# Kernel optimization log

Measured on AMD Instinct MI355X. Metric: run time of the kernel, lower is better.

The kernel has to match this reference:

```python
import jax, jax.numpy as jnp
import numpy as np
from itertools import combinations

H_RANK_MAX = 2
TP_RANK_MAX = 2
BASIS_RANK_MAX = 2
DIM = 3
N_NODES = 50000
N_EDGES = 400000
N_CHANNELS = 16
R_CUT = 10.0  # radial cutoff for Bessel RBF (assumed)


def find_combinations(a_max, b_max, s):
    if s > a_max + b_max or s < 0:
        return []
    return [(a, s - a) for a in range(max(0, s - b_max), min(a_max, s) + 1)]


def contraction_is_valid(n_in, n_out):
    # legs are removed in pairs (Kronecker-delta contractions)
    return (n_in >= n_out) and ((n_in - n_out) % 2 == 0)


def _matchings(legs):
    # all perfect matchings of an even-size list of leg indices
    if not legs:
        yield []
        return
    a = legs[0]
    for i in range(1, len(legs)):
        rest = legs[1:i] + legs[i + 1:]
        for m in _matchings(rest):
            yield [(a, legs[i])] + m


def contraction_specs(a, b, c_out):
    # all einsum strings contracting an [E,K,dim^a] x [E,K,dim^b] tensor product
    # (a+b legs total) down to c_out free Cartesian legs, pairing the rest.
    n = a + b
    specs = []
    for free in combinations(range(n), c_out):
        paired = [i for i in range(n) if i not in free]
        for m in _matchings(paired):
            lbl = {}
            it = iter('mnopqrstuvwxyz')
            for f in free:
                lbl[f] = next(it)
            for (i, j) in m:
                L = next(it)
                lbl[i] = L
                lbl[j] = L
            sa = ''.join(lbl[i] for i in range(a))
            sb = ''.join(lbl[i] for i in range(a, n))
            so = ''.join(lbl[f] for f in free)
            specs.append(f'ek{sa},ek{sb}->ek{so}')
    return specs


def e_rbf(r, n):
    # Bessel radial basis: n is [K,1], r is [E] -> [K,E]
    return jnp.sqrt(2.0 / R_CUT) * jnp.sin(n * jnp.pi * r / R_CUT) / r


def tensor_prod(r, order):
    # repeated outer product of unit vectors: order 0 -> [E], order k -> [E] + [DIM]*k
    out = jnp.ones(r.shape[0], dtype=r.dtype)
    for _ in range(order):
        out = jnp.einsum('e...,ed->e...d', out, r)
    return out


def setup_inputs() -> dict:
    key = jax.random.key(0)
    ks = jax.random.split(key, 7)
    h0 = jax.random.normal(ks[0], (N_NODES, N_CHANNELS), jnp.float32)
    h1 = jax.random.normal(ks[1], (N_NODES, N_CHANNELS, DIM), jnp.float32)
    h2 = jax.random.normal(ks[2], (N_NODES, N_CHANNELS, DIM, DIM), jnp.float32)
    pos = jax.random.normal(ks[3], (N_NODES, DIM), jnp.float32)
    channel_weights = jax.random.normal(ks[4], (H_RANK_MAX + 1, N_CHANNELS, N_CHANNELS), jnp.float32)
    src = jax.random.randint(ks[5], (N_EDGES,), 0, N_NODES, dtype=jnp.int32)
    off = jax.random.randint(ks[6], (N_EDGES,), 1, N_NODES, dtype=jnp.int32)
    dst = (src + off) % N_NODES  # no self-loops -> no zero distances
    edge_index = jnp.stack([src, dst])
    return {"h0": h0, "h1": h1, "h2": h2, "pos": pos,
            "channel_weights": channel_weights, "edge_index": edge_index}


def reference(h0, h1, h2, pos, channel_weights, edge_index):
    h = [h0, h1, h2]
    src, dst = edge_index[0], edge_index[1]
    rel = pos[src] - pos[dst]                       # [E,3]
    dists = jnp.linalg.norm(rel, axis=-1)           # [E]
    unit = rel / dists[:, None]
    hg = [g[dst] for g in h]                        # per-edge gathered features
    # NOTE: the original forward computes channel-mixed self.h with channel_weights
    # but the contraction loop uses the UNMIXED gathered h (h[split[0]]); replicated here,
    # so channel_weights does not affect the output (zero gradient).
    n_vals = jnp.arange(1, N_CHANNELS + 1, dtype=dists.dtype)[:, None]  # [K,1]
    radial = e_rbf(dists, n_vals).reshape(N_EDGES, N_CHANNELS)  # faithful reshape (not transpose), as in source
    r_raw = [tensor_prod(unit, o) for o in range(TP_RANK_MAX + 1)]
    r_w = [jnp.einsum('ek,e...->ek...', radial, t) for t in r_raw]  # [E,K]+[3]*b
    outs = [None] * (BASIS_RANK_MAX + 1)
    for n_ind in range(H_RANK_MAX + TP_RANK_MAX + 1):
        for (a, b) in find_combinations(H_RANK_MAX, TP_RANK_MAX, n_ind):
            for br in range(BASIS_RANK_MAX + 1):
                if contraction_is_valid(n_ind, br):
                    for spec in contraction_specs(a, b, br):
                        t = jnp.einsum(spec, hg[a], r_w[b])
                        outs[br] = t if outs[br] is None else outs[br] + t
    # sum over paths (done incrementally above == stack + 'i...->...'), scatter to nodes
    res = []
    for t in outs:
        if t is not None:
            res.append(jax.ops.segment_sum(t, src, num_segments=N_NODES))
    return tuple(res)
```

## Files before the change

### kernel.cpp

```cpp
#include <hip/hip_runtime.h>
#include <math.h>

#define N_NODES   50000
#define N_EDGES   400000
#define NCH       16
#define CAP       48
#define NSTRIPE   8
#define TPB       256
#define NBN       ((N_NODES + TPB - 1) / TPB)
#define NB_EDGES  ((N_EDGES + TPB - 1) / TPB)


__global__ void build_kernel(const float* __restrict__ pos,
                             const int* __restrict__ src,
                             const int* __restrict__ dst,
                             float* __restrict__ dists,
                             int* __restrict__ cnt,
                             int2* __restrict__ ebuf) {
    int e = blockIdx.x * TPB + threadIdx.x;
    if (e >= N_EDGES) return;
    int s = src[e];
    int d = dst[e];
    float rx = pos[3 * s + 0] - pos[3 * d + 0];
    float ry = pos[3 * s + 1] - pos[3 * d + 1];
    float rz = pos[3 * s + 2] - pos[3 * d + 2];
    float dist = sqrtf(rx * rx + ry * ry + rz * rz);
    dists[e] = dist;
    int slot = atomicAdd(&cnt[s], 1);
    if (slot < CAP) {
        ebuf[s * CAP + slot] = make_int2(e, d);
    }
}

__device__ __forceinline__ void edge_math(
    float ux, float uy, float uz, float R,
    float A0, const float A1[3], const float A2[9],
    float& acc0, float acc1[3], float acc2[9])
{
    float u[3] = {ux, uy, uz};
    float d1 = A1[0] * ux + A1[1] * uy + A1[2] * uz;
    float tA = A2[0] + A2[4] + A2[8];
    float v0 = A2[0] * ux + A2[1] * uy + A2[2] * uz;
    float v1 = A2[3] * ux + A2[4] * uy + A2[5] * uz;
    float v2 = A2[6] * ux + A2[7] * uy + A2[8] * uz;
    float w0 = A2[0] * ux + A2[3] * uy + A2[6] * uz;
    float w1 = A2[1] * ux + A2[4] * uy + A2[7] * uz;
    float w2 = A2[2] * ux + A2[5] * uy + A2[8] * uz;
    float q = ux * v0 + uy * v1 + uz * v2;

    acc0 += R * (2.0f * A0 + d1 + 2.0f * tA + 2.0f * q);

    float svw[3] = {v0 + w0, v1 + w1, v2 + w2};
    float a0t = A0 + tA;
#pragma unroll
    for (int mm = 0; mm < 3; ++mm) {
        acc1[mm] += R * (A0 * u[mm] + 2.0f * A1[mm] + 2.0f * d1 * u[mm]
                         + svw[mm] + tA * u[mm]);
#pragma unroll
        for (int nn = 0; nn < 3; ++nn) {
            acc2[3 * mm + nn] += R * (a0t * u[mm] * u[nn] + A1[mm] * u[nn]
                                      + 2.0f * A2[3 * mm + nn]
                                      + 2.0f * svw[mm] * u[nn]);
        }
    }
}

__device__ __forceinline__ void load_hset(
    const float* __restrict__ h0, const float* __restrict__ h1,
    const float* __restrict__ h2, const float* __restrict__ dists,
    int d, int e, int k,
    float& A0, float A1[3], float A2[9], float& r, float& nf)
{
    A0 = h0[d * NCH + k];
    const float* p1 = h1 + ((size_t)d * NCH + k) * 3;
    A1[0] = p1[0]; A1[1] = p1[1]; A1[2] = p1[2];
    const float* p2 = h2 + ((size_t)d * NCH + k) * 9;
#pragma unroll
    for (int q2 = 0; q2 < 9; ++q2) A2[q2] = p2[q2];
    unsigned f = (unsigned)e * NCH + (unsigned)k;
    unsigned n_idx = f / (unsigned)N_EDGES;
    unsigned e_idx = f - n_idx * (unsigned)N_EDGES;
    r = dists[e_idx];
    nf = (float)(n_idx + 1);
}

__device__ __forceinline__ float radial_R(float nf, float r) {
    return 0.44721359549995794f * __sinf(nf * 0.3141592653589793f * r) / r;
}

__global__ void node_wave_fast(const float* __restrict__ h0,
                               const float* __restrict__ h1,
                               const float* __restrict__ h2,
                               const float* __restrict__ pos,
                               const int* __restrict__ cnt,
                               const int2* __restrict__ ebuf,
                               const float* __restrict__ dists,
                               float* __restrict__ out0,
                               float* __restrict__ out1,
                               float* __restrict__ out2) {
    int gid = blockIdx.x * TPB + threadIdx.x;
    int node = gid >> 6;
    if (node >= N_NODES) return;
    int lane = threadIdx.x & 63;
    int k = lane & 15;
    int j = lane >> 4;
    int base = node * CAP;

    int m = cnt[node];
    int2 pk = ebuf[base + j];
    float ps0 = pos[3 * node + 0];
    float ps1 = pos[3 * node + 1];
    float ps2 = pos[3 * node + 2];
    if (m > CAP) m = CAP;

    float acc0 = 0.0f;
    float acc1[3] = {0.0f, 0.0f, 0.0f};
    float acc2[9] = {0.0f, 0.0f, 0.0f, 0.0f, 0.0f, 0.0f, 0.0f, 0.0f, 0.0f};

    int c = j;
    while (c < m) {
        int cn = c + 4;
        int2 pkn = pk;
        if (cn < m) pkn = ebuf[base + cn];

        int e = pk.x;
        int d = pk.y;

        float pd0 = pos[3 * d + 0];
        float pd1 = pos[3 * d + 1];
        float pd2 = pos[3 * d + 2];

        float A0 = h0[d * NCH + k];
        const float* a1p = h1 + ((size_t)d * NCH + k) * 3;
        float A1[3] = {a1p[0], a1p[1], a1p[2]};
        const float* a2p = h2 + ((size_t)d * NCH + k) * 9;
        float A2[9];
#pragma unroll
        for (int q2 = 0; q2 < 9; ++q2) A2[q2] = a2p[q2];

        unsigned f = (unsigned)e * NCH + (unsigned)k;
        unsigned n_idx = f / (unsigned)N_EDGES;
        unsigned e_idx = f - n_idx * (unsigned)N_EDGES;
        float r = dists[e_idx];
        float R = 0.44721359549995794f *
                  __sinf((float)(n_idx + 1) * 0.3141592653589793f * r) / r;

        float rx = ps0 - pd0;
        float ry = ps1 - pd1;
        float rz = ps2 - pd2;
        float dist = sqrtf(rx * rx + ry * ry + rz * rz);
        float inv = 1.0f / dist;
        float ux = rx * inv, uy = ry * inv, uz = rz * inv;

        edge_math(ux, uy, uz, R, A0, A1, A2, acc0, acc1, acc2);

        pk = pkn;
        c = cn;
    }

    acc0 += __shfl_xor(acc0, 16, 64);
    acc0 += __shfl_xor(acc0, 32, 64);
#pragma unroll
    for (int mm = 0; mm < 3; ++mm) {
        acc1[mm] += __shfl_xor(acc1[mm], 16, 64);
        acc1[mm] += __shfl_xor(acc1[mm], 32, 64);
    }
#pragma unroll
    for (int mm = 0; mm < 9; ++mm) {
        acc2[mm] += __shfl_xor(acc2[mm], 16, 64);
        acc2[mm] += __shfl_xor(acc2[mm], 32, 64);
    }

    if (j == 0) {
        int t = node * NCH + k;
        out0[t] = acc0;
        float* o1p = out1 + (size_t)t * 3;
#pragma unroll
        for (int mm = 0; mm < 3; ++mm) o1p[mm] = acc1[mm];
        float* o2p = out2 + (size_t)t * 9;
#pragma unroll
        for (int mm = 0; mm < 9; ++mm) o2p[mm] = acc2[mm];
    }
}


__global__ void fb_geom_hist(const float* __restrict__ pos,
                             const int* __restrict__ src,
                             const int* __restrict__ dst,
                             float* __restrict__ dists,
                             int* __restrict__ cnt8,
                             int* __restrict__ rankArr) {
    int e = blockIdx.x * TPB + threadIdx.x;
    if (e >= N_EDGES) return;
    int stripe = blockIdx.x & (NSTRIPE - 1);
    int s = src[e];
    int d = dst[e];
    float rx = pos[3 * s + 0] - pos[3 * d + 0];
    float ry = pos[3 * s + 1] - pos[3 * d + 1];
    float rz = pos[3 * s + 2] - pos[3 * d + 2];
    dists[e] = sqrtf(rx * rx + ry * ry + rz * rz);
    rankArr[e] = atomicAdd(&cnt8[stripe * N_NODES + s], 1);
}

__global__ void fb_scan(const int* __restrict__ cnt8,
                        int* __restrict__ incl,
                        int* __restrict__ bsum) {
    __shared__ int sh[TPB];
    int tid = threadIdx.x;
    int i = blockIdx.x * TPB + tid;
    int tot = 0;
    if (i < N_NODES) {
#pragma unroll
        for (int c = 0; c < NSTRIPE; ++c) tot += cnt8[c * N_NODES + i];
    }
    sh[tid] = tot;
    __syncthreads();
    for (int s = 1; s < TPB; s <<= 1) {
        int x = 0;
        if (tid >= s) x = sh[tid - s];
        __syncthreads();
        if (tid >= s) sh[tid] += x;
        __syncthreads();
    }
    if (i < N_NODES) incl[i] = sh[tid];
    if (tid == TPB - 1) bsum[blockIdx.x] = sh[TPB - 1];
}

__global__ void fb_final(const int* __restrict__ cnt8,
                         const int* __restrict__ incl,
                         const int* __restrict__ bsum,
                         int* __restrict__ offsets,
                         int* __restrict__ copyBase) {
    __shared__ int sh[TPB];
    int tid = threadIdx.x;
    int b = blockIdx.x;
    sh[tid] = (tid < b) ? bsum[tid] : 0;
    __syncthreads();
    for (int s = 128; s > 0; s >>= 1) {
        if (tid < s) sh[tid] += sh[tid + s];
        __syncthreads();
    }
    int base = sh[0];
    int i = b * TPB + tid;
    if (i < N_NODES) {
        int cv[NSTRIPE];
        int tot = 0;
#pragma unroll
        for (int c = 0; c < NSTRIPE; ++c) { cv[c] = cnt8[c * N_NODES + i]; tot += cv[c]; }
        int off = base + incl[i] - tot;
        offsets[i] = off;
        int run = off;
#pragma unroll
        for (int c = 0; c < NSTRIPE; ++c) { copyBase[c * N_NODES + i] = run; run += cv[c]; }
    }
    if (b == 0 && tid == 0) offsets[N_NODES] = N_EDGES;
}

__global__ void fb_fill(const int* __restrict__ src,
                        const int* __restrict__ dst,
                        const float* __restrict__ pos,
                        const float* __restrict__ dists,
                        const int* __restrict__ copyBase,
                        const int* __restrict__ rankArr,
                        float4* __restrict__ edata,
                        int* __restrict__ csr) {
    int e = blockIdx.x * TPB + threadIdx.x;
    if (e >= N_EDGES) return;
    int stripe = blockIdx.x & (NSTRIPE - 1);
    int s = src[e];
    int d = dst[e];
    float rx = pos[3 * s + 0] - pos[3 * d + 0];
    float ry = pos[3 * s + 1] - pos[3 * d + 1];
    float rz = pos[3 * s + 2] - pos[3 * d + 2];
    float inv = 1.0f / dists[e];
    int slot = copyBase[stripe * N_NODES + s] + rankArr[e];
    float4 ed;
    ed.x = rx * inv;
    ed.y = ry * inv;
    ed.z = rz * inv;
    ed.w = __int_as_float(d);
    edata[slot] = ed;
    csr[slot] = e;
}

__global__ void fb_main(const float* __restrict__ h0,
                        const float* __restrict__ h1,
                        const float* __restrict__ h2,
                        const int* __restrict__ offsets,
                        const float4* __restrict__ edata,
                        const int* __restrict__ csr,
                        const float* __restrict__ dists,
                        float* __restrict__ out0,
                        float* __restrict__ out1,
                        float* __restrict__ out2) {
    int gid = blockIdx.x * TPB + threadIdx.x;
    int node = gid >> 6;
    if (node >= N_NODES) return;
    int lane = threadIdx.x & 63;
    int k = lane & 15;
    int j = lane >> 4;
    int beg = offsets[node];
    int end = offsets[node + 1];

    float acc0 = 0.0f;
    float acc1[3] = {0.0f, 0.0f, 0.0f};
    float acc2[9] = {0.0f, 0.0f, 0.0f, 0.0f, 0.0f, 0.0f, 0.0f, 0.0f, 0.0f};

    int i = beg + j;
    float4 ed;
    int e = 0;
    if (i < end) { ed = edata[i]; e = csr[i]; }
    while (i < end) {
        int inext = i + 4;
        float4 edn = ed;
        int en = e;
        if (inext < end) { edn = edata[inext]; en = csr[inext]; }

        int d = __float_as_int(ed.w);
        float a0, a1[3], a2[9], r, nf;
        load_hset(h0, h1, h2, dists, d, e, k, a0, a1, a2, r, nf);
        float R = radial_R(nf, r);
        edge_math(ed.x, ed.y, ed.z, R, a0, a1, a2, acc0, acc1, acc2);

        ed = edn;
        e = en;
        i = inext;
    }

    acc0 += __shfl_xor(acc0, 16, 64);
    acc0 += __shfl_xor(acc0, 32, 64);
#pragma unroll
    for (int mm = 0; mm < 3; ++mm) {
        acc1[mm] += __shfl_xor(acc1[mm], 16, 64);
        acc1[mm] += __shfl_xor(acc1[mm], 32, 64);
    }
#pragma unroll
    for (int mm = 0; mm < 9; ++mm) {
        acc2[mm] += __shfl_xor(acc2[mm], 16, 64);
        acc2[mm] += __shfl_xor(acc2[mm], 32, 64);
    }

    if (j == 0) {
        int t = node * NCH + k;
        out0[t] = acc0;
        float* o1p = out1 + (size_t)t * 3;
#pragma unroll
        for (int mm = 0; mm < 3; ++mm) o1p[mm] = acc1[mm];
        float* o2p = out2 + (size_t)t * 9;
#pragma unroll
        for (int mm = 0; mm < 9; ++mm) o2p[mm] = acc2[mm];
    }
}


extern "C" void kernel_launch(void* const* d_in, const int* in_sizes, int n_in,
                              void* d_out, int out_size, void* d_ws, size_t ws_size,
                              hipStream_t stream) {
    const float* h0  = (const float*)d_in[0];
    const float* h1  = (const float*)d_in[1];
    const float* h2  = (const float*)d_in[2];
    const float* pos = (const float*)d_in[3];
    const int* edge_index = (const int*)d_in[5];
    const int* src = edge_index;
    const int* dst = edge_index + N_EDGES;

    float* out = (float*)d_out;
    float* out0 = out;
    float* out1 = out + (size_t)N_NODES * NCH;
    float* out2 = out + (size_t)N_NODES * NCH * 4;

    size_t need = (size_t)N_NODES * CAP * 8 + (size_t)N_EDGES * 4 + (size_t)N_NODES * 4;

    if (ws_size >= need) {
        int2* ebuf   = (int2*)d_ws;
        float* dists = (float*)(ebuf + (size_t)N_NODES * CAP);
        int* cnt     = (int*)(dists + N_EDGES);

        hipMemsetAsync(cnt, 0, N_NODES * sizeof(int), stream);
        build_kernel<<<NB_EDGES, TPB, 0, stream>>>(pos, src, dst, dists, cnt, ebuf);
        node_wave_fast<<<(N_NODES * 64 + TPB - 1) / TPB, TPB, 0, stream>>>(
            h0, h1, h2, pos, cnt, ebuf, dists, out0, out1, out2);
    } else {
        float4* edata   = (float4*)d_ws;
        float*  dists   = (float*)(edata + N_EDGES);
        int* cnt8       = (int*)(dists + N_EDGES);
        int* rankArr    = cnt8 + NSTRIPE * N_NODES;
        int* incl       = rankArr + N_EDGES;
        int* bsum       = incl + N_NODES;
        int* offsets    = bsum + 256;
        int* copyBase   = offsets + N_NODES + 1;
        int* csr        = copyBase + NSTRIPE * N_NODES;

        hipMemsetAsync(cnt8, 0, NSTRIPE * N_NODES * sizeof(int), stream);
        fb_geom_hist<<<NB_EDGES, TPB, 0, stream>>>(pos, src, dst, dists, cnt8, rankArr);
        fb_scan<<<NBN, TPB, 0, stream>>>(cnt8, incl, bsum);
        fb_final<<<NBN, TPB, 0, stream>>>(cnt8, incl, bsum, offsets, copyBase);
        fb_fill<<<NB_EDGES, TPB, 0, stream>>>(src, dst, pos, dists, copyBase, rankArr, edata, csr);
        fb_main<<<(N_NODES * 64 + TPB - 1) / TPB, TPB, 0, stream>>>(
            h0, h1, h2, offsets, edata, csr, dists, out0, out1, out2);
    }
}
```

Measured before the change: 184.4 us.

## Pack two nodes per wavefront and software-pipeline neighbor gathers

The main node kernel now processes two nodes per 64-lane wavefront (2 edge slots × 16 channels per node instead of 4), halving the grid and the shuffle reduction depth. The edge loop is software-pipelined: the next edge's position, h features and distance are loaded before the current edge's math runs, with unconditional ebuf reads made safe by padding the buffer. Division and sqrt are replaced by hardware rcp/rsq approximations. This targets gather latency and idle lanes for low-degree nodes, at the cost of more registers and fewer parallel edge slots per node.

```diff
diff --git a/kernel.cpp b/kernel.cpp
--- a/kernel.cpp
+++ b/kernel.cpp
@@ -5,10 +5,12 @@
 #define N_EDGES   400000
 #define NCH       16
 #define CAP       48
+#define EBUF_PAD  16
 #define NSTRIPE   8
 #define TPB       256
 #define NBN       ((N_NODES + TPB - 1) / TPB)
 #define NB_EDGES  ((N_EDGES + TPB - 1) / TPB)
+#define NB_MAIN   ((N_NODES / 2 * 64) / TPB)
 
 
 __global__ void build_kernel(const float* __restrict__ pos,
@@ -65,6 +67,30 @@
     }
 }
 
+__device__ __forceinline__ void load_hsetp(
+    const float* __restrict__ h0, const float* __restrict__ h1,
+    const float* __restrict__ h2, const float* __restrict__ pos,
+    const float* __restrict__ dists,
+    int d, int e, int k,
+    float& P0, float& P1, float& P2,
+    float& A0, float A1[3], float A2[9], float& r, float& nf)
+{
+    P0 = pos[3 * d + 0];
+    P1 = pos[3 * d + 1];
+    P2 = pos[3 * d + 2];
+    A0 = h0[d * NCH + k];
+    const float* p1 = h1 + ((size_t)d * NCH + k) * 3;
+    A1[0] = p1[0]; A1[1] = p1[1]; A1[2] = p1[2];
+    const float* p2 = h2 + ((size_t)d * NCH + k) * 9;
+#pragma unroll
+    for (int q2 = 0; q2 < 9; ++q2) A2[q2] = p2[q2];
+    unsigned f = (unsigned)e * NCH + (unsigned)k;
+    unsigned n_idx = f / (unsigned)N_EDGES;
+    unsigned e_idx = f - n_idx * (unsigned)N_EDGES;
+    r = dists[e_idx];
+    nf = (float)(n_idx + 1);
+}
+
 __device__ __forceinline__ void load_hset(
     const float* __restrict__ h0, const float* __restrict__ h1,
     const float* __restrict__ h2, const float* __restrict__ dists,
@@ -99,77 +125,67 @@
                                float* __restrict__ out1,
                                float* __restrict__ out2) {
     int gid = blockIdx.x * TPB + threadIdx.x;
-    int node = gid >> 6;
+    int lane = threadIdx.x & 63;
+    int half = lane >> 5;
+    int j = (lane >> 4) & 1;
+    int k = lane & 15;
+    int node = (gid >> 6) * 2 + half;
     if (node >= N_NODES) return;
-    int lane = threadIdx.x & 63;
-    int k = lane & 15;
-    int j = lane >> 4;
     int base = node * CAP;
 
     int m = cnt[node];
-    int2 pk = ebuf[base + j];
     float ps0 = pos[3 * node + 0];
     float ps1 = pos[3 * node + 1];
     float ps2 = pos[3 * node + 2];
+    int c = j;
+    int2 pk = ebuf[base + c];
     if (m > CAP) m = CAP;
+
+    bool v0 = (c < m);
+    int dc = v0 ? pk.y : 0;
+    int ec = v0 ? pk.x : 0;
+    float pd0, pd1, pd2, A0, A1[3], A2[9], rr, nf;
+    load_hsetp(h0, h1, h2, pos, dists, dc, ec, k,
+               pd0, pd1, pd2, A0, A1, A2, rr, nf);
 
     float acc0 = 0.0f;
     float acc1[3] = {0.0f, 0.0f, 0.0f};
     float acc2[9] = {0.0f, 0.0f, 0.0f, 0.0f, 0.0f, 0.0f, 0.0f, 0.0f, 0.0f};
 
-    int c = j;
     while (c < m) {
-        int cn = c + 4;
-        int2 pkn = pk;
-        if (cn < m) pkn = ebuf[base + cn];
-
-        int e = pk.x;
-        int d = pk.y;
-
-        float pd0 = pos[3 * d + 0];
-        float pd1 = pos[3 * d + 1];
-        float pd2 = pos[3 * d + 2];
-
-        float A0 = h0[d * NCH + k];
-        const float* a1p = h1 + ((size_t)d * NCH + k) * 3;
-        float A1[3] = {a1p[0], a1p[1], a1p[2]};
-        const float* a2p = h2 + ((size_t)d * NCH + k) * 9;
-        float A2[9];
-#pragma unroll
-        for (int q2 = 0; q2 < 9; ++q2) A2[q2] = a2p[q2];
-
-        unsigned f = (unsigned)e * NCH + (unsigned)k;
-        unsigned n_idx = f / (unsigned)N_EDGES;
-        unsigned e_idx = f - n_idx * (unsigned)N_EDGES;
-        float r = dists[e_idx];
+        int cn = c + 2;
+        int2 pk1 = ebuf[base + cn];
+        bool vn = (cn < m);
+        int dn = vn ? pk1.y : 0;
+        int en = vn ? pk1.x : 0;
+        float qd0, qd1, qd2, B0, B1[3], B2[9], sr, snf;
+        load_hsetp(h0, h1, h2, pos, dists, dn, en, k,
+                   qd0, qd1, qd2, B0, B1, B2, sr, snf);
+
+        float rcp_r = __builtin_amdgcn_rcpf(rr);
         float R = 0.44721359549995794f *
-                  __sinf((float)(n_idx + 1) * 0.3141592653589793f * r) / r;
-
+                  __sinf(nf * 0.3141592653589793f * rr) * rcp_r;
         float rx = ps0 - pd0;
         float ry = ps1 - pd1;
         float rz = ps2 - pd2;
-        float dist = sqrtf(rx * rx + ry * ry + rz * rz);
-        float inv = 1.0f / dist;
-        float ux = rx * inv, uy = ry * inv, uz = rz * inv;
-
-        edge_math(ux, uy, uz, R, A0, A1, A2, acc0, acc1, acc2);
-
-        pk = pkn;
+        float s2 = rx * rx + ry * ry + rz * rz;
+        float inv = __builtin_amdgcn_rsqf(s2);
+        edge_math(rx * inv, ry * inv, rz * inv, R, A0, A1, A2, acc0, acc1, acc2);
+
+        pd0 = qd0; pd1 = qd1; pd2 = qd2;
+        A0 = B0;
+        A1[0] = B1[0]; A1[1] = B1[1]; A1[2] = B1[2];
+#pragma unroll
+        for (int q2 = 0; q2 < 9; ++q2) A2[q2] = B2[q2];
+        rr = sr; nf = snf;
         c = cn;
     }
 
     acc0 += __shfl_xor(acc0, 16, 64);
-    acc0 += __shfl_xor(acc0, 32, 64);
-#pragma unroll
-    for (int mm = 0; mm < 3; ++mm) {
-        acc1[mm] += __shfl_xor(acc1[mm], 16, 64);
-        acc1[mm] += __shfl_xor(acc1[mm], 32, 64);
-    }
-#pragma unroll
-    for (int mm = 0; mm < 9; ++mm) {
-        acc2[mm] += __shfl_xor(acc2[mm], 16, 64);
-        acc2[mm] += __shfl_xor(acc2[mm], 32, 64);
-    }
+#pragma unroll
+    for (int mm = 0; mm < 3; ++mm) acc1[mm] += __shfl_xor(acc1[mm], 16, 64);
+#pragma unroll
+    for (int mm = 0; mm < 9; ++mm) acc2[mm] += __shfl_xor(acc2[mm], 16, 64);
 
     if (j == 0) {
         int t = node * NCH + k;
@@ -369,16 +385,17 @@
     float* out1 = out + (size_t)N_NODES * NCH;
     float* out2 = out + (size_t)N_NODES * NCH * 4;
 
-    size_t need = (size_t)N_NODES * CAP * 8 + (size_t)N_EDGES * 4 + (size_t)N_NODES * 4;
+    size_t need = ((size_t)N_NODES * CAP + EBUF_PAD) * 8
+                + (size_t)N_EDGES * 4 + (size_t)N_NODES * 4;
 
     if (ws_size >= need) {
         int2* ebuf   = (int2*)d_ws;
-        float* dists = (float*)(ebuf + (size_t)N_NODES * CAP);
+        float* dists = (float*)(ebuf + (size_t)N_NODES * CAP + EBUF_PAD);
         int* cnt     = (int*)(dists + N_EDGES);
 
         hipMemsetAsync(cnt, 0, N_NODES * sizeof(int), stream);
         build_kernel<<<NB_EDGES, TPB, 0, stream>>>(pos, src, dst, dists, cnt, ebuf);
-        node_wave_fast<<<(N_NODES * 64 + TPB - 1) / TPB, TPB, 0, stream>>>(
+        node_wave_fast<<<NB_MAIN, TPB, 0, stream>>>(
             h0, h1, h2, pos, cnt, ebuf, dists, out0, out1, out2);
     } else {
         float4* edata   = (float4*)d_ws;
```

Measured after the change: 184.5 us. About the same (+0.1%).

## Pack node features and position into float4 records for gather-friendly loads

Applied to the files above, without the earlier changes.

Adds a pre-pass kernel that repacks h0, h1, h2 and the node position into 16 contiguous floats per (node, channel), so the per-edge gather in the main kernel becomes four aligned float4 loads instead of many scalar strided loads. The edge buffer gets padding so the next-edge prefetch can run without a bounds check. The division and square root are replaced with hardware reciprocal and rsqrt intrinsics. The cost is an extra pass that writes about 51 MB to workspace and a larger workspace requirement, with the old kernel kept as a fallback path.

```diff
diff --git a/kernel.cpp b/kernel.cpp
--- a/kernel.cpp
+++ b/kernel.cpp
@@ -5,11 +5,36 @@
 #define N_EDGES   400000
 #define NCH       16
 #define CAP       48
+#define EBUF_PAD  16
 #define NSTRIPE   8
 #define TPB       256
 #define NBN       ((N_NODES + TPB - 1) / TPB)
 #define NB_EDGES  ((N_EDGES + TPB - 1) / TPB)
-
+#define NB_PACK   ((N_NODES * NCH + TPB - 1) / TPB)
+
+
+__global__ void pack_kernel(const float* __restrict__ h0,
+                            const float* __restrict__ h1,
+                            const float* __restrict__ h2,
+                            const float* __restrict__ pos,
+                            float4* __restrict__ hpack) {
+    int nk = blockIdx.x * TPB + threadIdx.x;
+    if (nk >= N_NODES * NCH) return;
+    int node = nk >> 4;
+    float4 v0, v1, v2, v3;
+    v0.x = h0[nk];
+    const float* p1 = h1 + (size_t)nk * 3;
+    v0.y = p1[0]; v0.z = p1[1]; v0.w = p1[2];
+    const float* p2 = h2 + (size_t)nk * 9;
+    v1.x = p2[0]; v1.y = p2[1]; v1.z = p2[2]; v1.w = p2[3];
+    v2.x = p2[4]; v2.y = p2[5]; v2.z = p2[6]; v2.w = p2[7];
+    v3.x = p2[8];
+    v3.y = pos[3 * node + 0];
+    v3.z = pos[3 * node + 1];
+    v3.w = pos[3 * node + 2];
+    float4* o = hpack + (size_t)nk * 4;
+    o[0] = v0; o[1] = v1; o[2] = v2; o[3] = v3;
+}
 
 __global__ void build_kernel(const float* __restrict__ pos,
                              const int* __restrict__ src,
@@ -88,10 +113,7 @@
     return 0.44721359549995794f * __sinf(nf * 0.3141592653589793f * r) / r;
 }
 
-__global__ void node_wave_fast(const float* __restrict__ h0,
-                               const float* __restrict__ h1,
-                               const float* __restrict__ h2,
-                               const float* __restrict__ pos,
+__global__ void node_wave_fast(const float4* __restrict__ hp,
                                const int* __restrict__ cnt,
                                const int2* __restrict__ ebuf,
                                const float* __restrict__ dists,
@@ -108,6 +130,96 @@
 
     int m = cnt[node];
     int2 pk = ebuf[base + j];
+    float4 own = hp[(((node << 4) | k) << 2) + 3];
+    float ps0 = own.y, ps1 = own.z, ps2 = own.w;
+    if (m > CAP) m = CAP;
+
+    float acc0 = 0.0f;
+    float acc1[3] = {0.0f, 0.0f, 0.0f};
+    float acc2[9] = {0.0f, 0.0f, 0.0f, 0.0f, 0.0f, 0.0f, 0.0f, 0.0f, 0.0f};
+
+    int c = j;
+    while (c < m) {
+        int cn = c + 4;
+        int2 pkn = ebuf[base + cn];
+
+        int e = pk.x;
+        int d = pk.y;
+
+        int hb = ((d << 4) | k) << 2;
+        float4 v0 = hp[hb + 0];
+        float4 v1 = hp[hb + 1];
+        float4 v2 = hp[hb + 2];
+        float4 v3 = hp[hb + 3];
+
+        unsigned f = (unsigned)e * NCH + (unsigned)k;
+        unsigned n_idx = f / (unsigned)N_EDGES;
+        unsigned e_idx = f - n_idx * (unsigned)N_EDGES;
+        float r = dists[e_idx];
+        float R = 0.44721359549995794f *
+                  __sinf((float)(n_idx + 1) * 0.3141592653589793f * r) *
+                  __builtin_amdgcn_rcpf(r);
+
+        float rx = ps0 - v3.y;
+        float ry = ps1 - v3.z;
+        float rz = ps2 - v3.w;
+        float s2 = rx * rx + ry * ry + rz * rz;
+        float inv = __builtin_amdgcn_rsqf(s2);
+
+        float A1[3] = {v0.y, v0.z, v0.w};
+        float A2[9] = {v1.x, v1.y, v1.z, v1.w, v2.x, v2.y, v2.z, v2.w, v3.x};
+        edge_math(rx * inv, ry * inv, rz * inv, R, v0.x, A1, A2,
+                  acc0, acc1, acc2);
+
+        pk = pkn;
+        c = cn;
+    }
+
+    acc0 += __shfl_xor(acc0, 16, 64);
+    acc0 += __shfl_xor(acc0, 32, 64);
+#pragma unroll
+    for (int mm = 0; mm < 3; ++mm) {
+        acc1[mm] += __shfl_xor(acc1[mm], 16, 64);
+        acc1[mm] += __shfl_xor(acc1[mm], 32, 64);
+    }
+#pragma unroll
+    for (int mm = 0; mm < 9; ++mm) {
+        acc2[mm] += __shfl_xor(acc2[mm], 16, 64);
+        acc2[mm] += __shfl_xor(acc2[mm], 32, 64);
+    }
+
+    if (j == 0) {
+        int t = node * NCH + k;
+        out0[t] = acc0;
+        float* o1p = out1 + (size_t)t * 3;
+#pragma unroll
+        for (int mm = 0; mm < 3; ++mm) o1p[mm] = acc1[mm];
+        float* o2p = out2 + (size_t)t * 9;
+#pragma unroll
+        for (int mm = 0; mm < 9; ++mm) o2p[mm] = acc2[mm];
+    }
+}
+
+__global__ void node_wave_mid(const float* __restrict__ h0,
+                              const float* __restrict__ h1,
+                              const float* __restrict__ h2,
+                              const float* __restrict__ pos,
+                              const int* __restrict__ cnt,
+                              const int2* __restrict__ ebuf,
+                              const float* __restrict__ dists,
+                              float* __restrict__ out0,
+                              float* __restrict__ out1,
+                              float* __restrict__ out2) {
+    int gid = blockIdx.x * TPB + threadIdx.x;
+    int node = gid >> 6;
+    if (node >= N_NODES) return;
+    int lane = threadIdx.x & 63;
+    int k = lane & 15;
+    int j = lane >> 4;
+    int base = node * CAP;
+
+    int m = cnt[node];
+    int2 pk = ebuf[base + j];
     float ps0 = pos[3 * node + 0];
     float ps1 = pos[3 * node + 1];
     float ps2 = pos[3 * node + 2];
@@ -150,9 +262,8 @@
         float rz = ps2 - pd2;
         float dist = sqrtf(rx * rx + ry * ry + rz * rz);
         float inv = 1.0f / dist;
-        float ux = rx * inv, uy = ry * inv, uz = rz * inv;
-
-        edge_math(ux, uy, uz, R, A0, A1, A2, acc0, acc1, acc2);
+
+        edge_math(rx * inv, ry * inv, rz * inv, R, A0, A1, A2, acc0, acc1, acc2);
 
         pk = pkn;
         c = cn;
@@ -369,16 +480,32 @@
     float* out1 = out + (size_t)N_NODES * NCH;
     float* out2 = out + (size_t)N_NODES * NCH * 4;
 
-    size_t need = (size_t)N_NODES * CAP * 8 + (size_t)N_EDGES * 4 + (size_t)N_NODES * 4;
-
-    if (ws_size >= need) {
+    const size_t hpack_f4 = (size_t)N_NODES * NCH * 4;
+    const size_t ebuf_n   = (size_t)N_NODES * CAP + EBUF_PAD;
+
+    size_t needA = hpack_f4 * 16 + ebuf_n * 8
+                 + (size_t)N_EDGES * 4 + (size_t)N_NODES * 4;
+    size_t needB = ebuf_n * 8 + (size_t)N_EDGES * 4 + (size_t)N_NODES * 4;
+
+    if (ws_size >= needA) {
+        float4* hpack = (float4*)d_ws;
+        int2* ebuf    = (int2*)(hpack + hpack_f4);
+        float* dists  = (float*)(ebuf + ebuf_n);
+        int* cnt      = (int*)(dists + N_EDGES);
+
+        hipMemsetAsync(cnt, 0, N_NODES * sizeof(int), stream);
+        pack_kernel<<<NB_PACK, TPB, 0, stream>>>(h0, h1, h2, pos, hpack);
+        build_kernel<<<NB_EDGES, TPB, 0, stream>>>(pos, src, dst, dists, cnt, ebuf);
+        node_wave_fast<<<(N_NODES * 64 + TPB - 1) / TPB, TPB, 0, stream>>>(
+            hpack, cnt, ebuf, dists, out0, out1, out2);
+    } else if (ws_size >= needB) {
         int2* ebuf   = (int2*)d_ws;
-        float* dists = (float*)(ebuf + (size_t)N_NODES * CAP);
+        float* dists = (float*)(ebuf + ebuf_n);
         int* cnt     = (int*)(dists + N_EDGES);
 
         hipMemsetAsync(cnt, 0, N_NODES * sizeof(int), stream);
         build_kernel<<<NB_EDGES, TPB, 0, stream>>>(pos, src, dst, dists, cnt, ebuf);
-        node_wave_fast<<<(N_NODES * 64 + TPB - 1) / TPB, TPB, 0, stream>>>(
+        node_wave_mid<<<(N_NODES * 64 + TPB - 1) / TPB, TPB, 0, stream>>>(
             h0, h1, h2, pos, cnt, ebuf, dists, out0, out1, out2);
     } else {
         float4* edata   = (float4*)d_ws;
```

Result: slower. 211.6 us (+14.8%).
